# Optimization experiments

Hardware: AMD Instinct MI355X
Metric: run time of the kernel (lower is better)

## Reference

```python
import jax, jax.numpy as jnp
import numpy as np

D_MODEL = 2048
N_HEADS = 16
HEAD_DIM = D_MODEL // N_HEADS  # 128
B, T = 2, 2048


def setup_inputs() -> dict:
    key = jax.random.key(0)
    ks = jax.random.split(key, 9)
    s = 0.02
    x = jax.random.normal(ks[0], (B, T, D_MODEL), dtype=jnp.float32)
    # Per-head projection weights (stacked over heads); torch Linear y = x @ W^T + b,
    # here W is stored as [H, d_model, head_dim] so y = einsum('btc,hcd->bhtd').
    Wq = jax.random.normal(ks[1], (N_HEADS, D_MODEL, HEAD_DIM), dtype=jnp.float32) * s
    bq = jax.random.normal(ks[2], (N_HEADS, HEAD_DIM), dtype=jnp.float32) * s
    Wk = jax.random.normal(ks[3], (N_HEADS, D_MODEL, HEAD_DIM), dtype=jnp.float32) * s
    bk = jax.random.normal(ks[4], (N_HEADS, HEAD_DIM), dtype=jnp.float32) * s
    Wv = jax.random.normal(ks[5], (N_HEADS, D_MODEL, HEAD_DIM), dtype=jnp.float32) * s
    bv = jax.random.normal(ks[6], (N_HEADS, HEAD_DIM), dtype=jnp.float32) * s
    Wo = jax.random.normal(ks[7], (D_MODEL, D_MODEL), dtype=jnp.float32) * s  # used as y @ Wo
    bo = jax.random.normal(ks[8], (D_MODEL,), dtype=jnp.float32) * s
    return {"x": x, "Wq": Wq, "bq": bq, "Wk": Wk, "bk": bk,
            "Wv": Wv, "bv": bv, "Wo": Wo, "bo": bo}


def reference(x, Wq, bq, Wk, bk, Wv, bv, Wo, bo):
    # x: [B, T, C]; per-head Q/K/V projections -> [B, H, T, D]
    Bn, Tn, C = x.shape
    H, _, D = Wq.shape
    scale = D ** (-0.5)
    q = jnp.einsum('btc,hcd->bhtd', x, Wq) + bq[None, :, None, :]
    k = jnp.einsum('btc,hcd->bhtd', x, Wk) + bk[None, :, None, :]
    v = jnp.einsum('btc,hcd->bhtd', x, Wv) + bv[None, :, None, :]
    # scores [B, H, T, T] with additive causal mask (finfo.min above the diagonal)
    scores = jnp.einsum('bhtd,bhsd->bhts', q, k) * scale
    neg = jnp.finfo(scores.dtype).min
    causal = jnp.triu(jnp.full((Tn, Tn), neg, dtype=scores.dtype), k=1)
    probs = jax.nn.softmax(scores + causal, axis=-1)
    y = jnp.einsum('bhts,bhsd->bhtd', probs, v)  # [B, H, T, D]
    # concat heads along feature dim (head order preserved) then output projection
    y = y.transpose(0, 2, 1, 3).reshape(Bn, Tn, H * D)
    return y @ Wo + bo
```

## Files before the change

### kernel.cpp

```cpp
#include <hip/hip_runtime.h>
#include <stdint.h>

typedef unsigned short u16;
typedef unsigned int u32;
typedef __attribute__((ext_vector_type(4))) u16 u16x4;
typedef __attribute__((ext_vector_type(8))) u16 u16x8;
typedef __attribute__((ext_vector_type(4))) u32 u32x4;
typedef __attribute__((ext_vector_type(8))) __bf16 bf16x8;
typedef __attribute__((ext_vector_type(4))) float f32x4;
typedef __attribute__((ext_vector_type(16))) float f32x16;

#define D_MODEL 2048
#define N_HEADS 16
#define HEAD_DIM 128
#define BATCH 2
#define SEQ 2048
#define M_TOT (BATCH*SEQ)
#define N_QKV (3*D_MODEL)

__device__ __forceinline__ u16 f2b(float f) {
  union { float f; uint32_t u; } c; c.f = f;
  uint32_t u = c.u;
  uint32_t r = (u + 0x7fffu + ((u >> 16) & 1u)) >> 16;
  return (u16)r;
}

__device__ __forceinline__ void gl_lds16(const u16* g, u16* l) {
  __builtin_amdgcn_global_load_lds(
      (const __attribute__((address_space(1))) uint32_t*)g,
      (__attribute__((address_space(3))) uint32_t*)l, 16, 0, 0);
}

template <int N> __device__ __forceinline__ void waitvm() {
  if constexpr (N == 7)      asm volatile("s_waitcnt vmcnt(7)" ::: "memory");
  else if constexpr (N == 6) asm volatile("s_waitcnt vmcnt(6)" ::: "memory");
  else if constexpr (N == 5) asm volatile("s_waitcnt vmcnt(5)" ::: "memory");
  else                       asm volatile("s_waitcnt vmcnt(0)" ::: "memory");
}
__device__ __forceinline__ void lgkm0() {
  asm volatile("s_waitcnt lgkmcnt(0)" ::: "memory");
}
__device__ __forceinline__ u32 cvtpk(float a, float b) {
  u32 r;
  asm("v_cvt_pk_bf16_f32 %0, %1, %2" : "=v"(r) : "v"(a), "v"(b));
  return r;
}

__global__ __launch_bounds__(256) void prep_kernel(
    const float* __restrict__ Wq, const float* __restrict__ Wk,
    const float* __restrict__ Wv, u16* __restrict__ Wt) {
  __shared__ u16 Tl[128][72];
  const int bid = blockIdx.x, tid = threadIdx.x;
  const int k0 = (bid & 31) * 64;
  const int hh = bid >> 5;
  const int qkv = hh >> 4, h = hh & 15;
  const float* src = (qkv == 0 ? Wq : qkv == 1 ? Wk : Wv) + (size_t)h * 2048 * 128;
  for (int it = 0; it < 32; ++it) {
    int idx = it * 256 + tid;
    int k = idx >> 7, d = idx & 127;
    Tl[d][k] = f2b(src[(size_t)(k0 + k) * 128 + d]);
  }
  __syncthreads();
  for (int it = 0; it < 32; ++it) {
    int idx = it * 256 + tid;
    int d = idx >> 6, kk = idx & 63;
    Wt[(size_t)(hh * 128 + d) * 2048 + k0 + kk] = Tl[d][kk];
  }
}

__global__ __launch_bounds__(256) void post_transpose_kernel(
    const float* __restrict__ Wo, u16* __restrict__ Wot,
    const u16* __restrict__ vb, u16* __restrict__ vt) {
  __shared__ u16 Tl[128 * 72];
  const int bid = blockIdx.x, tid = threadIdx.x;
  if (bid < 512) {
    const int k0 = (bid & 31) * 64;
    const int n0 = (bid >> 5) * 128;
    for (int it = 0; it < 32; ++it) {
      int idx = it * 256 + tid;
      int k = idx >> 7, n = idx & 127;
      Tl[n * 72 + k] = f2b(Wo[(size_t)(k0 + k) * 2048 + n0 + n]);
    }
    __syncthreads();
    for (int it = 0; it < 32; ++it) {
      int idx = it * 256 + tid;
      int d = idx >> 6, kk = idx & 63;
      Wot[(size_t)(n0 + d) * 2048 + k0 + kk] = Tl[d * 72 + kk];
    }
    return;
  }
  const int rel = bid - 512;
  const int t0 = (rel & 31) * 64;
  const int bh = rel >> 5;
  const u16* src = vb + (size_t)bh * 2048 * 128;
  u16* dstp = vt + (size_t)bh * 128 * 2048;
#pragma unroll
  for (int c = 0; c < 4; ++c) {
    int ci = c * 256 + tid;
    int tr = ci >> 4, d0 = (ci & 15) * 8;
    u16x8 v = *(const u16x8*)(src + (size_t)(t0 + tr) * 128 + d0);
#pragma unroll
    for (int e = 0; e < 8; ++e) Tl[(d0 + e) * 72 + tr] = v[e];
  }
  __syncthreads();
#pragma unroll
  for (int it = 0; it < 32; ++it) {
    int idx = it * 256 + tid;
    int d = idx >> 6, tt = idx & 63;
    dstp[(size_t)d * 2048 + t0 + ((tt & 15) * 4 + (tt >> 4))] = Tl[d * 72 + tt];
  }
}

__global__ __launch_bounds__(512, 2) void gemm_qkv_kernel(
    const float* __restrict__ X, const u16* __restrict__ B,
    u16* __restrict__ qo, u16* __restrict__ ko, u16* __restrict__ vo,
    const float* __restrict__ bq, const float* __restrict__ bk, const float* __restrict__ bv) {
  __shared__ u16 LS[3][20480];
  const int bid0 = blockIdx.x;
  const int gid = (bid0 & 7) * 32 + (bid0 >> 3);
  const int G = gid >> 4, l = gid & 15;
  const int m0 = ((G & 3) * 4 + (l & 3)) * 256;
  const int n0 = ((G >> 2) * 4 + (l >> 2)) * 384;

  const int tid = threadIdx.x, lane = tid & 63, w = tid >> 6;
  const int wm = (w >> 2) * 128, wn = (w & 3) * 96;
  const int l31 = lane & 31, g2 = lane >> 5;

  int aoff[2], boff[3];
#pragma unroll
  for (int l2 = 0; l2 < 2; ++l2) {
    int ci = l2 * 512 + tid, t = ci >> 3, x = (ci & 7) ^ (t & 7);
    aoff[l2] = (m0 + 2 * t + (x >> 2)) * 2048 + (x & 3) * 8;
  }
#pragma unroll
  for (int l2 = 0; l2 < 3; ++l2) {
    int ci = l2 * 512 + tid, t = ci >> 3, x = (ci & 7) ^ (t & 7);
    boff[l2] = (n0 + 2 * t + (x >> 2)) * 2048 + (x & 3) * 8;
  }
  const int adl = tid * 8;
  const int bdl = 8192 + tid * 8;

  f32x16 acc[4][3];
#pragma unroll
  for (int ai = 0; ai < 4; ++ai)
#pragma unroll
    for (int bj = 0; bj < 3; ++bj)
#pragma unroll
      for (int e = 0; e < 16; ++e) acc[ai][bj][e] = 0.f;

  f32x4 t0a = *(const f32x4*)(X + aoff[0]);
  f32x4 t0b = *(const f32x4*)(X + aoff[0] + 4);
  f32x4 t1a = *(const f32x4*)(X + aoff[1]);
  f32x4 t1b = *(const f32x4*)(X + aoff[1] + 4);
  f32x4 rc0a = *(const f32x4*)(X + aoff[0] + 32);
  f32x4 rc0b = *(const f32x4*)(X + aoff[0] + 36);
  f32x4 rc1a = *(const f32x4*)(X + aoff[1] + 32);
  f32x4 rc1b = *(const f32x4*)(X + aoff[1] + 36);
#pragma unroll
  for (int t = 0; t < 2; ++t)
#pragma unroll
    for (int l2 = 0; l2 < 3; ++l2)
      gl_lds16(B + boff[l2] + t * 32, LS[t] + bdl + l2 * 4096);
  {
    u32x4 w0 = {cvtpk(t0a[0], t0a[1]), cvtpk(t0a[2], t0a[3]),
                cvtpk(t0b[0], t0b[1]), cvtpk(t0b[2], t0b[3])};
    u32x4 w1 = {cvtpk(t1a[0], t1a[1]), cvtpk(t1a[2], t1a[3]),
                cvtpk(t1b[0], t1b[1]), cvtpk(t1b[2], t1b[3])};
    *(__shared__ u32x4*)(LS[0] + adl) = w0;
    *(__shared__ u32x4*)(LS[0] + adl + 4096) = w1;
  }
  waitvm<5>();
  lgkm0();
  __builtin_amdgcn_s_barrier();

  int s = 0;
  for (int kt = 0; kt < 64; ++kt) {
    const int sw = (s == 2) ? 0 : s + 1;
    f32x4 rn0a, rn0b, rn1a, rn1b;
    if (kt < 62) {
      const int s2 = (s == 0) ? 2 : s - 1;
      const int k2 = (kt + 2) * 32;
      rn0a = *(const f32x4*)(X + aoff[0] + k2);
      rn0b = *(const f32x4*)(X + aoff[0] + k2 + 4);
      rn1a = *(const f32x4*)(X + aoff[1] + k2);
      rn1b = *(const f32x4*)(X + aoff[1] + k2 + 4);
#pragma unroll
      for (int l2 = 0; l2 < 3; ++l2) gl_lds16(B + boff[l2] + k2, LS[s2] + bdl + l2 * 4096);
    }
    if (kt < 63) {
      u32x4 w0 = {cvtpk(rc0a[0], rc0a[1]), cvtpk(rc0a[2], rc0a[3]),
                  cvtpk(rc0b[0], rc0b[1]), cvtpk(rc0b[2], rc0b[3])};
      u32x4 w1 = {cvtpk(rc1a[0], rc1a[1]), cvtpk(rc1a[2], rc1a[3]),
                  cvtpk(rc1b[0], rc1b[1]), cvtpk(rc1b[2], rc1b[3])};
      *(__shared__ u32x4*)(LS[sw] + adl) = w0;
      *(__shared__ u32x4*)(LS[sw] + adl + 4096) = w1;
    }
    const char* base = (const char*)LS[s];
#pragma unroll
    for (int kk = 0; kk < 2; ++kk) {
      bf16x8 af[4];
#pragma unroll
      for (int ai = 0; ai < 4; ++ai) {
        int r = wm + ai * 32 + l31;
        int x = ((r & 1) << 2) | (2 * kk + g2);
        af[ai] = *(const bf16x8*)(base + (r >> 1) * 128 + 16 * (x ^ ((r >> 1) & 7)));
      }
      __builtin_amdgcn_s_setprio(1);
#pragma unroll
      for (int bj = 0; bj < 3; ++bj) {
        int rb = wn + bj * 32 + l31;
        int xb2 = ((rb & 1) << 2) | (2 * kk + g2);
        bf16x8 bfr = *(const bf16x8*)(base + 16384 + (rb >> 1) * 128 + 16 * (xb2 ^ ((rb >> 1) & 7)));
#pragma unroll
        for (int ai = 0; ai < 4; ++ai)
          acc[ai][bj] = __builtin_amdgcn_mfma_f32_32x32x16_bf16(af[ai], bfr, acc[ai][bj], 0, 0, 0);
      }
      __builtin_amdgcn_s_setprio(0);
    }
    if (kt < 62)       waitvm<7>();
    else if (kt == 62) waitvm<0>();
    lgkm0();
    __builtin_amdgcn_s_barrier();
    rc0a = rn0a; rc0b = rn0b; rc1a = rn1a; rc1b = rn1b;
    s = sw;
  }

  const float qscale = 0.08838834764831845f * 1.4426950408889634f;
#pragma unroll
  for (int bj = 0; bj < 3; ++bj) {
    const int n = n0 + wn + bj * 32 + l31;
    const int qkv = n >> 11, hh = (n >> 7) & 15, d = n & 127;
    const float* bias = (qkv == 0) ? bq : (qkv == 1) ? bk : bv;
    u16* dst = (qkv == 0) ? qo : (qkv == 1) ? ko : vo;
    const float bv_ = bias[n & 2047];
#pragma unroll
    for (int ai = 0; ai < 4; ++ai)
#pragma unroll
      for (int e = 0; e < 16; ++e) {
        int row = (e & 3) + 8 * (e >> 2) + 4 * g2;
        int gm = m0 + wm + ai * 32 + row;
        float val = acc[ai][bj][e] + bv_;
        if (qkv == 0) val *= qscale;
        int b = gm >> 11, t = gm & 2047;
        dst[((size_t)(b * 16 + hh) * 2048 + t) * 128 + d] = f2b(val);
      }
  }
}

__global__ __launch_bounds__(512, 2) void gemm_out_kernel(
    const u16* __restrict__ A, const u16* __restrict__ B,
    float* __restrict__ outf, const float* __restrict__ bo) {
  __shared__ u16 LS[3][24576];
  const int bid0 = blockIdx.x;
  const int gid = (bid0 & 7) * 32 + (bid0 >> 3);
  const int G = gid >> 4, l = gid & 15;
  const int m0 = ((G & 3) * 4 + (l & 3)) * 256;
  const int n0 = ((G >> 2) * 4 + (l >> 2)) * 128;

  const int tid = threadIdx.x, lane = tid & 63, w = tid >> 6;
  const int wm = (w >> 1) * 64, wn = (w & 1) * 64;
  const int lr = lane & 15, g = lane >> 4;
  const int kx = (lr & 7) << 4;

  int aoff[4], boff[2];
#pragma unroll
  for (int l2 = 0; l2 < 4; ++l2) {
    int ci = l2 * 512 + tid, r = ci >> 3, gj = ci & 7;
    aoff[l2] = (m0 + r) * 2048 + (gj ^ (r & 7)) * 8;
  }
#pragma unroll
  for (int l2 = 0; l2 < 2; ++l2) {
    int ci = l2 * 512 + tid, r = ci >> 3, gj = ci & 7;
    boff[l2] = (n0 + r) * 2048 + (gj ^ (r & 7)) * 8;
  }
  const int adl = tid * 8;
  const int bdl = 16384 + tid * 8;

  f32x4 acc[4][4];
  const f32x4 zero = {0.f, 0.f, 0.f, 0.f};
#pragma unroll
  for (int ai = 0; ai < 4; ++ai)
#pragma unroll
    for (int bj = 0; bj < 4; ++bj) acc[ai][bj] = zero;

#pragma unroll
  for (int t = 0; t < 2; ++t) {
#pragma unroll
    for (int l2 = 0; l2 < 4; ++l2) gl_lds16(A + aoff[l2] + t * 64, LS[t] + adl + l2 * 4096);
#pragma unroll
    for (int l2 = 0; l2 < 2; ++l2) gl_lds16(B + boff[l2] + t * 64, LS[t] + bdl + l2 * 4096);
  }
  waitvm<6>();
  __builtin_amdgcn_s_barrier();

  int s = 0;
  for (int kt = 0; kt < 32; ++kt) {
    if (kt < 30) {
      const int s2 = (s == 0) ? 2 : s - 1;
      const int k2 = (kt + 2) * 64;
#pragma unroll
      for (int l2 = 0; l2 < 4; ++l2) gl_lds16(A + aoff[l2] + k2, LS[s2] + adl + l2 * 4096);
#pragma unroll
      for (int l2 = 0; l2 < 2; ++l2) gl_lds16(B + boff[l2] + k2, LS[s2] + bdl + l2 * 4096);
    }
    const char* base = (const char*)LS[s];
#pragma unroll
    for (int h = 0; h < 2; ++h) {
      bf16x8 af[4];
#pragma unroll
      for (int ai = 0; ai < 4; ++ai) {
        int r = wm + ai * 16 + lr;
        af[ai] = *(const bf16x8*)(base + r * 128 + ((h * 64 + 16 * g) ^ kx));
      }
      __builtin_amdgcn_s_setprio(1);
#pragma unroll
      for (int bj = 0; bj < 4; ++bj) {
        int rb = wn + bj * 16 + lr;
        bf16x8 bfr = *(const bf16x8*)(base + 32768 + rb * 128 + ((h * 64 + 16 * g) ^ kx));
#pragma unroll
        for (int ai = 0; ai < 4; ++ai)
          acc[ai][bj] = __builtin_amdgcn_mfma_f32_16x16x32_bf16(af[ai], bfr, acc[ai][bj], 0, 0, 0);
      }
      __builtin_amdgcn_s_setprio(0);
    }
    if (kt < 30)       waitvm<6>();
    else if (kt == 30) waitvm<0>();
    __builtin_amdgcn_s_barrier();
    s = (s == 2) ? 0 : s + 1;
  }

  const int rbase = g * 4;
#pragma unroll
  for (int bj = 0; bj < 4; ++bj) {
    const int gn = n0 + wn + bj * 16 + lr;
    const float bv_ = bo[gn];
#pragma unroll
    for (int ai = 0; ai < 4; ++ai)
#pragma unroll
      for (int r = 0; r < 4; ++r) {
        int gm = m0 + wm + ai * 16 + rbase + r;
        outf[(size_t)gm * 2048 + gn] = acc[ai][bj][r] + bv_;
      }
  }
}

__global__ __launch_bounds__(256) void attn_kernel(
    const u16* __restrict__ qg, const u16* __restrict__ kg,
    const u16* __restrict__ vtg, u16* __restrict__ y) {
  __shared__ u16 Kb[2][64 * 128];
  __shared__ u16 Vb[2][128 * 64];
  __shared__ u16 Pl[4][32 * 64];
  const int tid = threadIdx.x, lane = tid & 63, w = tid >> 6;
  const int bid = blockIdx.x;
  const int bh = bid & 31, qt = 15 - (bid >> 5);
  const int b = bh >> 4, h = bh & 15;
  const int lr = lane & 15, lk = (lane >> 4) * 8;
  const u16* Qp = qg + (size_t)bh * (2048 * 128);
  const u16* Kp = kg + (size_t)bh * (2048 * 128);
  const u16* Vp = vtg + (size_t)bh * (128 * 2048);

  int koff[4], voff[4], dstc[4];
#pragma unroll
  for (int c = 0; c < 4; ++c) {
    int ci = c * 256 + tid;
    dstc[c] = ci * 8;
    int kr = ci >> 4, kj = ci & 15;
    koff[c] = kr * 128 + (kj ^ (kr & 7)) * 8;
    int vd = ci >> 3, vj = ci & 7;
    voff[c] = vd * 2048 + (vj ^ (vd & 7)) * 8;
  }
  const int kxor = (lr & 7) << 4;
  const int rbase = (lane >> 4) * 4;
  const f32x4 zero = {0.f, 0.f, 0.f, 0.f};

  const int q0 = qt * 128;
  const int qw = q0 + w * 32;
  const int nt = 2 * qt + 2;

  bf16x8 qf[2][4];
#pragma unroll
  for (int s = 0; s < 2; ++s)
#pragma unroll
    for (int i = 0; i < 4; ++i)
      qf[s][i] = *(const bf16x8*)(Qp + (size_t)(qw + s * 16 + lr) * 128 + i * 32 + lk);

  f32x4 o[2][8];
#pragma unroll
  for (int s = 0; s < 2; ++s)
#pragma unroll
    for (int f = 0; f < 8; ++f) o[s][f] = zero;
  float mrow[2][4], lrow[2][4];
#pragma unroll
  for (int s = 0; s < 2; ++s)
#pragma unroll
    for (int r = 0; r < 4; ++r) { mrow[s][r] = -1e30f; lrow[s][r] = 0.f; }

#pragma unroll
  for (int c = 0; c < 4; ++c) gl_lds16(Kp + koff[c], Kb[0] + dstc[c]);
#pragma unroll
  for (int c = 0; c < 4; ++c) gl_lds16(Vp + voff[c], Vb[0] + dstc[c]);
  __syncthreads();

  int cur = 0;
  for (int t = 0; t < nt; ++t) {
    const int s0 = t * 64;
    if (t + 1 < nt) {
      const size_t skn = (size_t)(s0 + 64) * 128;
#pragma unroll
      for (int c = 0; c < 4; ++c) gl_lds16(Kp + skn + koff[c], Kb[cur ^ 1] + dstc[c]);
#pragma unroll
      for (int c = 0; c < 4; ++c) gl_lds16(Vp + (s0 + 64) + voff[c], Vb[cur ^ 1] + dstc[c]);
    }
    if (s0 <= qw + 31) {
      const char* Kc = (const char*)Kb[cur];
      f32x4 sf[2][4];
      __builtin_amdgcn_s_setprio(1);
#pragma unroll
      for (int sj = 0; sj < 4; ++sj) {
        f32x4 a0 = zero, a1 = zero;
#pragma unroll
        for (int i = 0; i < 4; ++i) {
          bf16x8 kf = *(const bf16x8*)(Kc + ((((sj * 16 + lr) * 256) + (i * 32 + lk) * 2) ^ kxor));
          a0 = __builtin_amdgcn_mfma_f32_16x16x32_bf16(qf[0][i], kf, a0, 0, 0, 0);
          a1 = __builtin_amdgcn_mfma_f32_16x16x32_bf16(qf[1][i], kf, a1, 0, 0, 0);
        }
        sf[0][sj] = a0; sf[1][sj] = a1;
      }
      __builtin_amdgcn_s_setprio(0);

      char* Pc = (char*)Pl[w];
      const bool diag = (s0 + 63 > qw);
      float pmax[2][4];
      bool need = false;
#pragma unroll
      for (int s = 0; s < 2; ++s)
#pragma unroll
        for (int r = 0; r < 4; ++r) {
          if (diag) {
            const int rq = qw + s * 16 + rbase + r;
#pragma unroll
            for (int sj = 0; sj < 4; ++sj)
              if (s0 + sj * 16 + lr > rq) sf[s][sj][r] = -1e30f;
          }
          float pm = fmaxf(fmaxf(sf[s][0][r], sf[s][1][r]),
                           fmaxf(sf[s][2][r], sf[s][3][r]));
          pmax[s][r] = pm;
          need |= (pm > mrow[s][r] + 8.f);
        }
      if (__any(need)) {
#pragma unroll
        for (int s = 0; s < 2; ++s)
#pragma unroll
          for (int r = 0; r < 4; ++r) {
            float pm = pmax[s][r];
            pm = fmaxf(pm, __shfl_xor(pm, 1));
            pm = fmaxf(pm, __shfl_xor(pm, 2));
            pm = fmaxf(pm, __shfl_xor(pm, 4));
            pm = fmaxf(pm, __shfl_xor(pm, 8));
            float mnew = fmaxf(mrow[s][r], pm);
            float sfac = __builtin_amdgcn_exp2f(mrow[s][r] - mnew);
            mrow[s][r] = mnew;
            lrow[s][r] *= sfac;
#pragma unroll
            for (int f = 0; f < 8; ++f) o[s][f][r] *= sfac;
          }
      }
#pragma unroll
      for (int s = 0; s < 2; ++s)
#pragma unroll
        for (int r = 0; r < 4; ++r) {
          const int prow = s * 16 + rbase + r;
          float p0 = __builtin_amdgcn_exp2f(sf[s][0][r] - mrow[s][r]);
          float p1 = __builtin_amdgcn_exp2f(sf[s][1][r] - mrow[s][r]);
          float p2 = __builtin_amdgcn_exp2f(sf[s][2][r] - mrow[s][r]);
          float p3 = __builtin_amdgcn_exp2f(sf[s][3][r] - mrow[s][r]);
          lrow[s][r] += (p0 + p1) + (p2 + p3);
          uint32_t lo = cvtpk(p0, p1), hi = cvtpk(p2, p3);
          uint32_t* pp = (uint32_t*)(Pc + ((prow * 128 + lr * 8) ^ ((prow & 7) << 4)));
          pp[0] = lo; pp[1] = hi;
        }

      const char* Vc = (const char*)Vb[cur];
      __builtin_amdgcn_s_setprio(1);
#pragma unroll
      for (int st = 0; st < 2; ++st) {
        bf16x8 pf0 = *(const bf16x8*)(Pc + (((lr * 128) + (st * 32 + lk) * 2) ^ kxor));
        bf16x8 pf1 = *(const bf16x8*)(Pc + ((((16 + lr) * 128) + (st * 32 + lk) * 2) ^ kxor));
#pragma unroll
        for (int f = 0; f < 8; ++f) {
          bf16x8 vf = *(const bf16x8*)(Vc + ((((f * 16 + lr) * 128) + (st * 32 + lk) * 2) ^ kxor));
          o[0][f] = __builtin_amdgcn_mfma_f32_16x16x32_bf16(pf0, vf, o[0][f], 0, 0, 0);
          o[1][f] = __builtin_amdgcn_mfma_f32_16x16x32_bf16(pf1, vf, o[1][f], 0, 0, 0);
        }
      }
      __builtin_amdgcn_s_setprio(0);
    }
    __syncthreads();
    cur ^= 1;
  }

#pragma unroll
  for (int s = 0; s < 2; ++s)
#pragma unroll
    for (int r = 0; r < 4; ++r) {
      float l = lrow[s][r];
      l += __shfl_xor(l, 1);
      l += __shfl_xor(l, 2);
      l += __shfl_xor(l, 4);
      l += __shfl_xor(l, 8);
      const float rinv = __builtin_amdgcn_rcpf(l);
      const int row = qw + s * 16 + rbase + r;
#pragma unroll
      for (int f = 0; f < 8; ++f)
        y[((size_t)b * 2048 + row) * 2048 + h * 128 + f * 16 + lr] =
            f2b(o[s][f][r] * rinv);
    }
}


extern "C" void kernel_launch(void* const* d_in, const int* in_sizes, int n_in,
                              void* d_out, int out_size, void* d_ws, size_t ws_size,
                              hipStream_t stream) {
  const float* x  = (const float*)d_in[0];
  const float* Wq = (const float*)d_in[1];
  const float* bq = (const float*)d_in[2];
  const float* Wk = (const float*)d_in[3];
  const float* bk = (const float*)d_in[4];
  const float* Wv = (const float*)d_in[5];
  const float* bv = (const float*)d_in[6];
  const float* Wo = (const float*)d_in[7];
  const float* bo = (const float*)d_in[8];
  float* out = (float*)d_out;
  char* ws = (char*)d_ws;

  u16* yb  = (u16*)(ws + 0);
  u16* Wt  = (u16*)(ws + 16777216);
  u16* qb  = (u16*)(ws + 41943040);
  u16* kb  = (u16*)(ws + 58720256);
  u16* vb  = (u16*)(ws + 75497472);
  u16* Wot = Wt;
  u16* vtb = (u16*)(ws + 25165824);

  prep_kernel<<<1536, 256, 0, stream>>>(Wq, Wk, Wv, Wt);
  gemm_qkv_kernel<<<256, 512, 0, stream>>>(x, Wt, qb, kb, vb, bq, bk, bv);
  post_transpose_kernel<<<1536, 256, 0, stream>>>(Wo, Wot, vb, vtb);
  attn_kernel<<<512, 256, 0, stream>>>(qb, kb, vtb, yb);
  gemm_out_kernel<<<256, 512, 0, stream>>>(yb, Wot, out, bo);
}
```

Baseline: 263.6 us.

## Shrink attention KV tile to 32 keys for better causal skipping and occupancy

Cuts the attention key/value tile from 64 to 32 keys. This halves the LDS buffers for K, V^T and P and adds a launch bound of 3 blocks per SM. The V transpose store order and the LDS swizzle patterns change to match the new 32-wide tiles. The aim is less wasted work on the causal diagonal and more resident blocks, at the cost of twice as many loop iterations, barriers and prefetches per block.

```diff
diff --git a/kernel.cpp b/kernel.cpp
--- a/kernel.cpp
+++ b/kernel.cpp
@@ -107,7 +107,8 @@
   for (int it = 0; it < 32; ++it) {
     int idx = it * 256 + tid;
     int d = idx >> 6, tt = idx & 63;
-    dstp[(size_t)d * 2048 + t0 + ((tt & 15) * 4 + (tt >> 4))] = Tl[d * 72 + tt];
+    int col = (tt & 32) | ((tt & 15) * 2 + ((tt >> 4) & 1));
+    dstp[(size_t)d * 2048 + t0 + col] = Tl[d * 72 + tt];
   }
 }
 
@@ -344,38 +345,40 @@
   }
 }
 
-__global__ __launch_bounds__(256) void attn_kernel(
+__global__ __launch_bounds__(256, 3) void attn_kernel(
     const u16* __restrict__ qg, const u16* __restrict__ kg,
     const u16* __restrict__ vtg, u16* __restrict__ y) {
-  __shared__ u16 Kb[2][64 * 128];
-  __shared__ u16 Vb[2][128 * 64];
-  __shared__ u16 Pl[4][32 * 64];
+  __shared__ u16 Kb[2][32 * 128];
+  __shared__ u16 Vb[2][128 * 32];
+  __shared__ u16 Pl[4][32 * 32];
   const int tid = threadIdx.x, lane = tid & 63, w = tid >> 6;
   const int bid = blockIdx.x;
   const int bh = bid & 31, qt = 15 - (bid >> 5);
   const int b = bh >> 4, h = bh & 15;
   const int lr = lane & 15, lk = (lane >> 4) * 8;
+  const int g16 = lane >> 4;
   const u16* Qp = qg + (size_t)bh * (2048 * 128);
   const u16* Kp = kg + (size_t)bh * (2048 * 128);
   const u16* Vp = vtg + (size_t)bh * (128 * 2048);
 
-  int koff[4], voff[4], dstc[4];
-#pragma unroll
-  for (int c = 0; c < 4; ++c) {
+  int koff[2], voff[2], kdst[2], vdst[2];
+#pragma unroll
+  for (int c = 0; c < 2; ++c) {
     int ci = c * 256 + tid;
-    dstc[c] = ci * 8;
+    kdst[c] = ci * 8;
     int kr = ci >> 4, kj = ci & 15;
     koff[c] = kr * 128 + (kj ^ (kr & 7)) * 8;
-    int vd = ci >> 3, vj = ci & 7;
-    voff[c] = vd * 2048 + (vj ^ (vd & 7)) * 8;
+    vdst[c] = ci * 8;
+    int vd = ci >> 2, vj = ci & 3;
+    voff[c] = vd * 2048 + (vj ^ ((vd >> 1) & 3)) * 8;
   }
   const int kxor = (lr & 7) << 4;
-  const int rbase = (lane >> 4) * 4;
+  const int rbase = g16 * 4;
   const f32x4 zero = {0.f, 0.f, 0.f, 0.f};
 
   const int q0 = qt * 128;
   const int qw = q0 + w * 32;
-  const int nt = 2 * qt + 2;
+  const int nt = 4 * qt + 4;
 
   bf16x8 qf[2][4];
 #pragma unroll
@@ -396,27 +399,27 @@
     for (int r = 0; r < 4; ++r) { mrow[s][r] = -1e30f; lrow[s][r] = 0.f; }
 
 #pragma unroll
-  for (int c = 0; c < 4; ++c) gl_lds16(Kp + koff[c], Kb[0] + dstc[c]);
-#pragma unroll
-  for (int c = 0; c < 4; ++c) gl_lds16(Vp + voff[c], Vb[0] + dstc[c]);
+  for (int c = 0; c < 2; ++c) gl_lds16(Kp + koff[c], Kb[0] + kdst[c]);
+#pragma unroll
+  for (int c = 0; c < 2; ++c) gl_lds16(Vp + voff[c], Vb[0] + vdst[c]);
   __syncthreads();
 
   int cur = 0;
   for (int t = 0; t < nt; ++t) {
-    const int s0 = t * 64;
+    const int s0 = t * 32;
     if (t + 1 < nt) {
-      const size_t skn = (size_t)(s0 + 64) * 128;
-#pragma unroll
-      for (int c = 0; c < 4; ++c) gl_lds16(Kp + skn + koff[c], Kb[cur ^ 1] + dstc[c]);
-#pragma unroll
-      for (int c = 0; c < 4; ++c) gl_lds16(Vp + (s0 + 64) + voff[c], Vb[cur ^ 1] + dstc[c]);
+      const size_t skn = (size_t)(s0 + 32) * 128;
+#pragma unroll
+      for (int c = 0; c < 2; ++c) gl_lds16(Kp + skn + koff[c], Kb[cur ^ 1] + kdst[c]);
+#pragma unroll
+      for (int c = 0; c < 2; ++c) gl_lds16(Vp + (s0 + 32) + voff[c], Vb[cur ^ 1] + vdst[c]);
     }
     if (s0 <= qw + 31) {
       const char* Kc = (const char*)Kb[cur];
-      f32x4 sf[2][4];
+      f32x4 sf[2][2];
       __builtin_amdgcn_s_setprio(1);
 #pragma unroll
-      for (int sj = 0; sj < 4; ++sj) {
+      for (int sj = 0; sj < 2; ++sj) {
         f32x4 a0 = zero, a1 = zero;
 #pragma unroll
         for (int i = 0; i < 4; ++i) {
@@ -429,7 +432,7 @@
       __builtin_amdgcn_s_setprio(0);
 
       char* Pc = (char*)Pl[w];
-      const bool diag = (s0 + 63 > qw);
+      const bool diag = (s0 + 31 > qw);
       float pmax[2][4];
       bool need = false;
 #pragma unroll
@@ -439,11 +442,10 @@
           if (diag) {
             const int rq = qw + s * 16 + rbase + r;
 #pragma unroll
-            for (int sj = 0; sj < 4; ++sj)
+            for (int sj = 0; sj < 2; ++sj)
               if (s0 + sj * 16 + lr > rq) sf[s][sj][r] = -1e30f;
           }
-          float pm = fmaxf(fmaxf(sf[s][0][r], sf[s][1][r]),
-                           fmaxf(sf[s][2][r], sf[s][3][r]));
+          float pm = fmaxf(sf[s][0][r], sf[s][1][r]);
           pmax[s][r] = pm;
           need |= (pm > mrow[s][r] + 8.f);
         }
@@ -472,23 +474,21 @@
           const int prow = s * 16 + rbase + r;
           float p0 = __builtin_amdgcn_exp2f(sf[s][0][r] - mrow[s][r]);
           float p1 = __builtin_amdgcn_exp2f(sf[s][1][r] - mrow[s][r]);
-          float p2 = __builtin_amdgcn_exp2f(sf[s][2][r] - mrow[s][r]);
-          float p3 = __builtin_amdgcn_exp2f(sf[s][3][r] - mrow[s][r]);
-          lrow[s][r] += (p0 + p1) + (p2 + p3);
-          uint32_t lo = cvtpk(p0, p1), hi = cvtpk(p2, p3);
-          uint32_t* pp = (uint32_t*)(Pc + ((prow * 128 + lr * 8) ^ ((prow & 7) << 4)));
-          pp[0] = lo; pp[1] = hi;
+          lrow[s][r] += p0 + p1;
+          u32 pk = cvtpk(p0, p1);
+          *(u32*)(Pc + ((prow * 64 + lr * 4) ^ (((prow >> 1) & 3) << 4))) = pk;
         }
 
       const char* Vc = (const char*)Vb[cur];
       __builtin_amdgcn_s_setprio(1);
-#pragma unroll
-      for (int st = 0; st < 2; ++st) {
-        bf16x8 pf0 = *(const bf16x8*)(Pc + (((lr * 128) + (st * 32 + lk) * 2) ^ kxor));
-        bf16x8 pf1 = *(const bf16x8*)(Pc + ((((16 + lr) * 128) + (st * 32 + lk) * 2) ^ kxor));
+      {
+        const int pr0 = lr, pr1 = 16 + lr;
+        bf16x8 pf0 = *(const bf16x8*)(Pc + ((pr0 * 64 + 16 * g16) ^ (((pr0 >> 1) & 3) << 4)));
+        bf16x8 pf1 = *(const bf16x8*)(Pc + ((pr1 * 64 + 16 * g16) ^ (((pr1 >> 1) & 3) << 4)));
 #pragma unroll
         for (int f = 0; f < 8; ++f) {
-          bf16x8 vf = *(const bf16x8*)(Vc + ((((f * 16 + lr) * 128) + (st * 32 + lk) * 2) ^ kxor));
+          const int vr = f * 16 + lr;
+          bf16x8 vf = *(const bf16x8*)(Vc + ((vr * 64 + 16 * g16) ^ (((vr >> 1) & 3) << 4)));
           o[0][f] = __builtin_amdgcn_mfma_f32_16x16x32_bf16(pf0, vf, o[0][f], 0, 0, 0);
           o[1][f] = __builtin_amdgcn_mfma_f32_16x16x32_bf16(pf1, vf, o[1][f], 0, 0, 0);
         }
```

After: 325.2 us. 1.23x slower.
